# Performance work log

Hardware: AMD Instinct MI355X
Metric: run time of the kernel (lower is better)

Reference implementation:

```python
import jax, jax.numpy as jnp
import numpy as np

B, C, H = 16, 256, 32          # batch, in_channels(=out_channels), image_size
HEADS, HS = 8, 32              # heads = out_channels // head_size
D = HEADS * HS                 # head_dim = 256
N = H * H                      # tokens = 1024
EPS = 1e-5


def _rel_indices(h, w):
    # Faithful port of RelativeAttention2d.get_indices
    y = np.arange(h)
    x = np.arange(w)
    y1, x1, y2, x2 = np.meshgrid(y, x, y, x, indexing='ij')
    idx = (y1 - y2 + h - 1) * (2 * w - 1) + (x1 - x2 + w - 1)
    return jnp.asarray(idx.reshape(-1), dtype=jnp.int32)  # [N*N]


def setup_inputs() -> dict:
    key = jax.random.key(0)
    ks = jax.random.split(key, 10)
    s = 0.02
    return {
        'x': jax.random.normal(ks[0], (B, C, H, H), jnp.float32),
        'ln_g': jnp.ones((C,), jnp.float32),
        'ln_b': jnp.zeros((C,), jnp.float32),
        'wq': jax.random.normal(ks[1], (D, C), jnp.float32) * s,
        'bq': jnp.zeros((D,), jnp.float32),
        'wk': jax.random.normal(ks[2], (D, C), jnp.float32) * s,
        'bk': jnp.zeros((D,), jnp.float32),
        'wv': jax.random.normal(ks[3], (D, C), jnp.float32) * s,
        'bv': jnp.zeros((D,), jnp.float32),
        'wo': jax.random.normal(ks[4], (C, D), jnp.float32) * s,
        'bo': jnp.zeros((C,), jnp.float32),
        'rel_bias': jax.random.normal(ks[5], (HEADS, (2 * H - 1) * (2 * H - 1)), jnp.float32),
        'rel_idx': _rel_indices(H, H),
    }


def reference(x, ln_g, ln_b, wq, bq, wk, bk, wv, bv, wo, bo, rel_bias, rel_idx):
    b = x.shape[0]
    # norm(): LayerNorm over channel axis (dim 1 after the double transpose)
    mu = jnp.mean(x, axis=1, keepdims=True)
    var = jnp.mean((x - mu) ** 2, axis=1, keepdims=True)
    xn = (x - mu) / jnp.sqrt(var + EPS)
    xn = xn * ln_g[None, :, None, None] + ln_b[None, :, None, None]
    # reshape_for_linear: raw reshape [b, C, H, W] -> [b, N, C] (as in torch)
    xr = xn.reshape(b, N, C)
    # projections, then raw view(b, heads, head_size, -1) as in torch
    q = (xr @ wq.T + bq).reshape(b, HEADS, HS, N)
    k = (xr @ wk.T + bk).reshape(b, HEADS, HS, N)
    v = (xr @ wv.T + bv).reshape(b, HEADS, HS, N)
    # dots = k^T q / sqrt(head_dim)   [b, heads, N, N]
    dots = jnp.einsum('bhdn,bhdm->bhnm', k, q) / np.float32(np.sqrt(D))
    # gathered relative position bias  [heads, N, N]
    bias = rel_bias[:, rel_idx].reshape(HEADS, N, N)
    attn = jax.nn.softmax(dots + bias[None], axis=-2)  # non-standard softmax dim
    # out = v @ attn  [b, heads, head_size, N]
    out = jnp.einsum('bhdn,bhnm->bhdm', v, attn)
    out = out.reshape(b, H, H, D)  # raw view as in torch
    out = out @ wo.T + bo          # to_output linear (dropout is identity in eval)
    out = out.reshape(b, C, H, H)  # raw view back to [b, out_channels, H, W]
    return x + out
```

## Files before the change

kernel.cpp:

```cpp
#include <hip/hip_runtime.h>
#include <cstdint>

#define PERB 262144

typedef __attribute__((ext_vector_type(8))) short bf16x8;
typedef __attribute__((ext_vector_type(4))) float f32x4;
typedef unsigned short ushort_t;

__device__ __forceinline__ uint16_t f2bf(float f) {
    uint32_t u = __float_as_uint(f);
    u += 0x7fff + ((u >> 16) & 1);
    return (uint16_t)(u >> 16);
}

__global__ __launch_bounds__(256) void wcvt_kernel(
    const float* __restrict__ wq, const float* __restrict__ wk,
    const float* __restrict__ wv, const float* __restrict__ wo,
    ushort_t* __restrict__ oq, ushort_t* __restrict__ ok,
    ushort_t* __restrict__ ov, ushort_t* __restrict__ oo)
{
    const int which = blockIdx.x >> 6;
    const int idx = ((blockIdx.x & 63) * 256 + threadIdx.x) * 4;
    const float* src = which == 0 ? wq : which == 1 ? wk : which == 2 ? wv : wo;
    ushort_t* dst    = which == 0 ? oq : which == 1 ? ok : which == 2 ? ov : oo;
    const float4 v = *(const float4*)&src[idx];
    uint2 p;
    p.x = (uint32_t)f2bf(v.x) | ((uint32_t)f2bf(v.y) << 16);
    p.y = (uint32_t)f2bf(v.z) | ((uint32_t)f2bf(v.w) << 16);
    *(uint2*)&dst[idx] = p;
}

__global__ __launch_bounds__(256) void ln_kernel(
    const float* __restrict__ x, const float* __restrict__ gam,
    const float* __restrict__ bet, ushort_t* __restrict__ X)
{
    const int blk = blockIdx.x;
    const int b   = blk >> 4;
    const int sp0 = (blk & 15) << 6;
    const int tid = threadIdx.x;
    const int spl = tid & 63;
    const int cg  = tid >> 6;
    const int c0  = cg << 6;
    const int sp  = sp0 + spl;
    const float* xb = x + (size_t)b * PERB + sp;

    float vals[64];
    float s = 0.f, sq = 0.f;
#pragma unroll
    for (int i = 0; i < 64; ++i) {
        float v = xb[(size_t)(c0 + i) * 1024];
        vals[i] = v; s += v; sq += v * v;
    }
    __shared__ float rs[4][64];
    __shared__ float rq[4][64];
    rs[cg][spl] = s; rq[cg][spl] = sq;
    __syncthreads();
    const float ts = rs[0][spl] + rs[1][spl] + rs[2][spl] + rs[3][spl];
    const float tq = rq[0][spl] + rq[1][spl] + rq[2][spl] + rq[3][spl];
    const float mean = ts * (1.f / 256.f);
    const float var  = tq * (1.f / 256.f) - mean * mean;
    const float rstd = rsqrtf(var + 1e-5f);

    ushort_t* Xb = X + (size_t)b * PERB + sp;
#pragma unroll
    for (int i = 0; i < 64; ++i) {
        const int c = c0 + i;
        Xb[(size_t)c * 1024] = f2bf((vals[i] - mean) * rstd * gam[c] + bet[c]);
    }
}

__global__ __launch_bounds__(256, 3) void qkv_kernel(
    const ushort_t* __restrict__ X,
    const ushort_t* __restrict__ wq, const float* __restrict__ bq,
    const ushort_t* __restrict__ wk, const float* __restrict__ bk,
    const ushort_t* __restrict__ wv, const float* __restrict__ bv,
    ushort_t* __restrict__ Q, ushort_t* __restrict__ K, ushort_t* __restrict__ V)
{
    __shared__ __align__(16) ushort_t Xl[512 * 8];
    __shared__ __align__(16) ushort_t Wl[3][512 * 8];

    const int blk = blockIdx.x;
    const int m0  = (blk >> 2) << 6;
    const int n0  = (blk & 3) << 6;
    const int tid = threadIdx.x;
    const int w    = tid >> 6;
    const int lane = tid & 63;
    const int quad = lane >> 4;
    const int c    = lane & 15;

    f32x4 acc[3][4];
#pragma unroll
    for (int o3 = 0; o3 < 3; ++o3)
#pragma unroll
        for (int i = 0; i < 4; ++i) acc[o3][i] = (f32x4){0.f, 0.f, 0.f, 0.f};

    for (int kc = 0; kc < 4; ++kc) {
        const int k0 = kc << 6;
        __syncthreads();
#pragma unroll
        for (int i = 0; i < 2; ++i) {
            const int id = tid + i * 256;
            const int kq = id >> 6, m = id & 63;
            *(bf16x8*)&Xl[id * 8] = *(const bf16x8*)&X[(size_t)(m0 + m) * 256 + k0 + kq * 8];
        }
#pragma unroll
        for (int i = 0; i < 2; ++i) {
            const int id = tid + i * 256;
            const int kq = id >> 6, n = id & 63;
            const size_t g = (size_t)(n0 + n) * 256 + k0 + kq * 8;
            *(bf16x8*)&Wl[0][id * 8] = *(const bf16x8*)&wq[g];
            *(bf16x8*)&Wl[1][id * 8] = *(const bf16x8*)&wk[g];
            *(bf16x8*)&Wl[2][id * 8] = *(const bf16x8*)&wv[g];
        }
        __syncthreads();
#pragma unroll
        for (int ks = 0; ks < 2; ++ks) {
            const int kq = ks * 4 + quad;
            bf16x8 af[4];
#pragma unroll
            for (int msub = 0; msub < 4; ++msub)
                af[msub] = *(const bf16x8*)&Xl[(kq * 64 + msub * 16 + c) * 8];
            bf16x8 bw[3];
#pragma unroll
            for (int o3 = 0; o3 < 3; ++o3)
                bw[o3] = *(const bf16x8*)&Wl[o3][(kq * 64 + w * 16 + c) * 8];
#pragma unroll
            for (int o3 = 0; o3 < 3; ++o3)
#pragma unroll
                for (int msub = 0; msub < 4; ++msub)
                    acc[o3][msub] = __builtin_amdgcn_mfma_f32_16x16x32_bf16(
                        bw[o3], af[msub], acc[o3][msub], 0, 0, 0);
        }
    }

    const int n = n0 + w * 16 + quad * 4;
    const float4 bq4 = *(const float4*)&bq[n];
    const float4 bk4 = *(const float4*)&bk[n];
    const float4 bv4 = *(const float4*)&bv[n];
    ushort_t* outs[3] = {Q, K, V};
    const float4 bias[3] = {bq4, bk4, bv4};
#pragma unroll
    for (int msub = 0; msub < 4; ++msub) {
        const size_t m = (size_t)(m0 + msub * 16 + c);
#pragma unroll
        for (int o3 = 0; o3 < 3; ++o3) {
            const f32x4 a = acc[o3][msub];
            uint2 p;
            p.x = (uint32_t)f2bf(a[0] + bias[o3].x) | ((uint32_t)f2bf(a[1] + bias[o3].y) << 16);
            p.y = (uint32_t)f2bf(a[2] + bias[o3].z) | ((uint32_t)f2bf(a[3] + bias[o3].w) << 16);
            *(uint2*)&outs[o3][m * 256 + n] = p;
        }
    }
}

#define C1F 0.09016844005556022f
#define LOG2EF 1.4426950408889634f

__global__ __launch_bounds__(256, 4) void attn_kernel(
    const ushort_t* __restrict__ Q, const ushort_t* __restrict__ K,
    const ushort_t* __restrict__ V, const float* __restrict__ relb,
    ushort_t* __restrict__ O)
{
    __shared__ __align__(16) unsigned char smem[28672];
    char* Pb = (char*)smem;
    char* Kl = (char*)(smem + 16384);
    char* Vl = (char*)(smem + 20480);

    const int blk = blockIdx.x;
    const int bh  = blk & 127;
    const int mt  = blk >> 7;
    const int b   = bh >> 3;
    const int h   = bh & 7;
    const int m0  = mt << 7;
    const int tid = threadIdx.x;
    const int w    = tid >> 6;
    const int lane = tid & 63;
    const int quad = lane >> 4;
    const int c    = lane & 15;

    const size_t base = (size_t)b * PERB + (size_t)h * 32768;
    const ushort_t* Qg = Q + base;
    const ushort_t* Kg = K + base;
    const ushort_t* Vg = V + base;
    const float* rbh = relb + h * 3969;

    {
        const int mm = tid & 127;
        const int sg = tid >> 7;
        union { bf16x8 v; uint16_t u[8]; } g0, g1;
#pragma unroll
        for (int j = 0; j < 8; ++j)
            g0.u[j] = Qg[(size_t)(sg * 16 + j) * 1024 + m0 + mm];
#pragma unroll
        for (int j = 0; j < 8; ++j)
            g1.u[j] = Qg[(size_t)(sg * 16 + 8 + j) * 1024 + m0 + mm];
        *(bf16x8*)(Pb + (sg * 2 + 0) * 2048 + mm * 16) = g0.v;
        *(bf16x8*)(Pb + (sg * 2 + 1) * 2048 + mm * 16) = g1.v;
    }
    __syncthreads();
    bf16x8 qfrag[8];
#pragma unroll
    for (int msub = 0; msub < 8; ++msub)
        qfrag[msub] = *(const bf16x8*)(Pb + quad * 2048 + (msub * 16 + c) * 16);

    int moff[8];
#pragma unroll
    for (int msub = 0; msub < 8; ++msub) {
        const int m = m0 + msub * 16 + c;
        moff[msub] = 1984 - (m >> 5) * 63 - (m & 31);
    }

    f32x4 oacc[2][2], dacc[2];
#pragma unroll
    for (int i = 0; i < 2; ++i) {
        dacc[i] = (f32x4){0.f, 0.f, 0.f, 0.f};
#pragma unroll
        for (int j = 0; j < 2; ++j) oacc[i][j] = (f32x4){0.f, 0.f, 0.f, 0.f};
    }
    bf16x8 onesf;
#pragma unroll
    for (int j = 0; j < 8; ++j) onesf[j] = (short)0x3F80;

    const int knn = tid & 63, ksg = tid >> 6;
    const int vs  = tid >> 3, vng = tid & 7;
    const int kWr = ksg * 1024 + knn * 16;
    const int vWr = vs * 128 + ((vng ^ (vs & 7)) << 4);
    const int kRd = quad * 1024 + (w * 16 + c) * 16;
    const int pWr = c * 128 + (((2 * w + (quad >> 1)) ^ (c & 7)) << 4) + ((quad & 1) << 3);
    const int c7  = c & 7;

    uint32_t kpre[8]; bf16x8 vpre;
#pragma unroll
    for (int j = 0; j < 8; ++j) kpre[j] = Kg[(size_t)(ksg * 8 + j) * 1024 + knn];
    vpre = *(const bf16x8*)&Vg[(size_t)vs * 1024 + vng * 8];

    for (int ch = 0; ch < 16; ++ch) {
        const int n0c = ch << 6;
        const int cb  = ch & 1;

        {
            uint4 kp;
            kp.x = kpre[0] | (kpre[1] << 16);
            kp.y = kpre[2] | (kpre[3] << 16);
            kp.z = kpre[4] | (kpre[5] << 16);
            kp.w = kpre[6] | (kpre[7] << 16);
            *(uint4*)(Kl + kWr) = kp;
            *(bf16x8*)(Vl + cb * 4096 + vWr) = vpre;
        }
        __syncthreads();

        {
            const int n0n = ((ch + 1) & 15) << 6;
#pragma unroll
            for (int j = 0; j < 8; ++j)
                kpre[j] = Kg[(size_t)(ksg * 8 + j) * 1024 + n0n + knn];
            vpre = *(const bf16x8*)&Vg[(size_t)vs * 1024 + n0n + vng * 8];
        }

        const bf16x8 kf = *(const bf16x8*)(Kl + kRd);
        f32x4 sacc[8];
#pragma unroll
        for (int msub = 0; msub < 8; ++msub) {
            const f32x4 z = {0.f, 0.f, 0.f, 0.f};
            sacc[msub] = __builtin_amdgcn_mfma_f32_16x16x32_bf16(kf, qfrag[msub], z, 0, 0, 0);
        }

        const int nbase = n0c + w * 16 + quad * 4;
        const int nidx0 = (nbase >> 5) * 63 + (nbase & 31);
#pragma unroll
        for (int msub = 0; msub < 8; ++msub) {
            const float* bp = rbh + nidx0 + moff[msub];
            float p[4];
#pragma unroll
            for (int r = 0; r < 4; ++r)
                p[r] = __builtin_amdgcn_exp2f(fmaf(bp[r], LOG2EF, sacc[msub][r] * C1F));
            uint2 pk;
            pk.x = __builtin_amdgcn_perm(__float_as_uint(p[1]), __float_as_uint(p[0]), 0x07060302u);
            pk.y = __builtin_amdgcn_perm(__float_as_uint(p[3]), __float_as_uint(p[2]), 0x07060302u);
            *(uint2*)(Pb + msub * 2048 + pWr) = pk;
        }
        __syncthreads();

#pragma unroll
        for (int kstep = 0; kstep < 2; ++kstep) {
            const int u = ((kstep * 4 + quad) ^ c7) << 4;
            const bf16x8 vf0 = *(const bf16x8*)(Vl + cb * 4096 + c * 128 + u);
            const bf16x8 vf1 = *(const bf16x8*)(Vl + cb * 4096 + (16 + c) * 128 + u);
#pragma unroll
            for (int mi = 0; mi < 2; ++mi) {
                const bf16x8 pf = *(const bf16x8*)(Pb + ((w * 2 + mi) * 16 + c) * 128 + u);
                oacc[0][mi] = __builtin_amdgcn_mfma_f32_16x16x32_bf16(vf0, pf, oacc[0][mi], 0, 0, 0);
                oacc[1][mi] = __builtin_amdgcn_mfma_f32_16x16x32_bf16(vf1, pf, oacc[1][mi], 0, 0, 0);
                dacc[mi]    = __builtin_amdgcn_mfma_f32_16x16x32_bf16(onesf, pf, dacc[mi], 0, 0, 0);
            }
        }
    }

    ushort_t* Ob = O + base;
#pragma unroll
    for (int mi = 0; mi < 2; ++mi) {
        const float inv = 1.0f / dacc[mi][0];
        const int m = m0 + (w * 2 + mi) * 16 + c;
#pragma unroll
        for (int ssub = 0; ssub < 2; ++ssub)
#pragma unroll
            for (int r = 0; r < 4; ++r)
                Ob[(size_t)(ssub * 16 + quad * 4 + r) * 1024 + m] = f2bf(oacc[ssub][mi][r] * inv);
    }
}

__global__ __launch_bounds__(256, 4) void oproj_kernel(
    const ushort_t* __restrict__ A, const ushort_t* __restrict__ wo,
    const float* __restrict__ bo, const float* __restrict__ x,
    float* __restrict__ out)
{
    __shared__ __align__(16) ushort_t Al[512 * 8];
    __shared__ __align__(16) ushort_t Wl[512 * 8];

    const int blk = blockIdx.x;
    const int m0  = (blk >> 2) << 6;
    const int n0  = (blk & 3) << 6;
    const int tid = threadIdx.x;
    const int w    = tid >> 6;
    const int lane = tid & 63;
    const int quad = lane >> 4;
    const int c    = lane & 15;

    f32x4 acc[4];
#pragma unroll
    for (int i = 0; i < 4; ++i) acc[i] = (f32x4){0.f, 0.f, 0.f, 0.f};

    for (int kc = 0; kc < 4; ++kc) {
        const int k0 = kc << 6;
        __syncthreads();
#pragma unroll
        for (int i = 0; i < 2; ++i) {
            const int id = tid + i * 256;
            const int kq = id >> 6, mn = id & 63;
            *(bf16x8*)&Al[id * 8] = *(const bf16x8*)&A [(size_t)(m0 + mn) * 256 + k0 + kq * 8];
            *(bf16x8*)&Wl[id * 8] = *(const bf16x8*)&wo[(size_t)(n0 + mn) * 256 + k0 + kq * 8];
        }
        __syncthreads();
#pragma unroll
        for (int ks = 0; ks < 2; ++ks) {
            const int kq = ks * 4 + quad;
            const bf16x8 bw = *(const bf16x8*)&Wl[(kq * 64 + w * 16 + c) * 8];
#pragma unroll
            for (int msub = 0; msub < 4; ++msub) {
                const bf16x8 af = *(const bf16x8*)&Al[(kq * 64 + msub * 16 + c) * 8];
                acc[msub] = __builtin_amdgcn_mfma_f32_16x16x32_bf16(bw, af, acc[msub], 0, 0, 0);
            }
        }
    }

    const int n = n0 + w * 16 + quad * 4;
    const float4 bo4 = *(const float4*)&bo[n];
#pragma unroll
    for (int msub = 0; msub < 4; ++msub) {
        const size_t g = (size_t)(m0 + msub * 16 + c) * 256 + n;
        const float4 r = *(const float4*)&x[g];
        float4 t;
        t.x = acc[msub][0] + bo4.x + r.x;
        t.y = acc[msub][1] + bo4.y + r.y;
        t.z = acc[msub][2] + bo4.z + r.z;
        t.w = acc[msub][3] + bo4.w + r.w;
        *(float4*)&out[g] = t;
    }
}

extern "C" void kernel_launch(void* const* d_in, const int* in_sizes, int n_in,
                              void* d_out, int out_size, void* d_ws, size_t ws_size,
                              hipStream_t stream)
{
    (void)in_sizes; (void)n_in; (void)out_size; (void)ws_size;
    const float* x   = (const float*)d_in[0];
    const float* lng = (const float*)d_in[1];
    const float* lnb = (const float*)d_in[2];
    const float* wq  = (const float*)d_in[3];
    const float* bq  = (const float*)d_in[4];
    const float* wk  = (const float*)d_in[5];
    const float* bk  = (const float*)d_in[6];
    const float* wv  = (const float*)d_in[7];
    const float* bv  = (const float*)d_in[8];
    const float* wo  = (const float*)d_in[9];
    const float* bo  = (const float*)d_in[10];
    const float* rb  = (const float*)d_in[11];

    ushort_t* ws = (ushort_t*)d_ws;
    ushort_t* Xbf = ws;
    ushort_t* Qbf = ws + 1 * 4194304;
    ushort_t* Kbf = ws + 2 * 4194304;
    ushort_t* Vbf = ws + 3 * 4194304;
    ushort_t* Obf = ws + 4 * 4194304;
    ushort_t* Wqb = ws + 5 * 4194304;
    ushort_t* Wkb = Wqb + 65536;
    ushort_t* Wvb = Wkb + 65536;
    ushort_t* Wob = Wvb + 65536;
    float* out = (float*)d_out;

    hipLaunchKernelGGL(wcvt_kernel,  dim3(256),  dim3(256), 0, stream,
                       wq, wk, wv, wo, Wqb, Wkb, Wvb, Wob);
    hipLaunchKernelGGL(ln_kernel,    dim3(256),  dim3(256), 0, stream, x, lng, lnb, Xbf);
    hipLaunchKernelGGL(qkv_kernel,   dim3(1024), dim3(256), 0, stream,
                       Xbf, Wqb, bq, Wkb, bk, Wvb, bv, Qbf, Kbf, Vbf);
    hipLaunchKernelGGL(attn_kernel,  dim3(1024), dim3(256), 0, stream, Qbf, Kbf, Vbf, rb, Obf);
    hipLaunchKernelGGL(oproj_kernel, dim3(1024), dim3(256), 0, stream, Obf, Wob, bo, x, out);
}
```

Before: 179.2 us.

## Merge weight-convert and layernorm kernels; halve attention query tile to double grid

Fuses the weight bf16 conversion and the layernorm into one prep kernel, saving a launch. The layernorm now uses 512 smaller blocks of 32 spatial positions × 8 channel groups, giving more parallelism. The attention kernel now handles 64 queries per block instead of 128, which doubles the grid to 2048 blocks and shrinks LDS and register use. The cost is that each K/V chunk is loaded and staged twice as often per query, and the per-chunk barriers are amortised over less MFMA work.

Measured after the change: 176.7 us. No clear change (-1.4%).

```diff
diff --git a/kernel.cpp b/kernel.cpp
--- a/kernel.cpp
+++ b/kernel.cpp
@@ -13,59 +13,60 @@
     return (uint16_t)(u >> 16);
 }
 
-__global__ __launch_bounds__(256) void wcvt_kernel(
+__global__ __launch_bounds__(256) void prep_kernel(
+    const float* __restrict__ x, const float* __restrict__ gam,
+    const float* __restrict__ bet, ushort_t* __restrict__ X,
     const float* __restrict__ wq, const float* __restrict__ wk,
     const float* __restrict__ wv, const float* __restrict__ wo,
     ushort_t* __restrict__ oq, ushort_t* __restrict__ ok,
     ushort_t* __restrict__ ov, ushort_t* __restrict__ oo)
 {
-    const int which = blockIdx.x >> 6;
-    const int idx = ((blockIdx.x & 63) * 256 + threadIdx.x) * 4;
-    const float* src = which == 0 ? wq : which == 1 ? wk : which == 2 ? wv : wo;
-    ushort_t* dst    = which == 0 ? oq : which == 1 ? ok : which == 2 ? ov : oo;
-    const float4 v = *(const float4*)&src[idx];
-    uint2 p;
-    p.x = (uint32_t)f2bf(v.x) | ((uint32_t)f2bf(v.y) << 16);
-    p.y = (uint32_t)f2bf(v.z) | ((uint32_t)f2bf(v.w) << 16);
-    *(uint2*)&dst[idx] = p;
-}
-
-__global__ __launch_bounds__(256) void ln_kernel(
-    const float* __restrict__ x, const float* __restrict__ gam,
-    const float* __restrict__ bet, ushort_t* __restrict__ X)
-{
     const int blk = blockIdx.x;
-    const int b   = blk >> 4;
-    const int sp0 = (blk & 15) << 6;
     const int tid = threadIdx.x;
-    const int spl = tid & 63;
-    const int cg  = tid >> 6;
-    const int c0  = cg << 6;
+    if (blk < 256) {
+        const int which = blk >> 6;
+        const int idx = ((blk & 63) * 256 + tid) * 4;
+        const float* src = which == 0 ? wq : which == 1 ? wk : which == 2 ? wv : wo;
+        ushort_t* dst    = which == 0 ? oq : which == 1 ? ok : which == 2 ? ov : oo;
+        const float4 v = *(const float4*)&src[idx];
+        uint2 p;
+        p.x = (uint32_t)f2bf(v.x) | ((uint32_t)f2bf(v.y) << 16);
+        p.y = (uint32_t)f2bf(v.z) | ((uint32_t)f2bf(v.w) << 16);
+        *(uint2*)&dst[idx] = p;
+        return;
+    }
+    const int lb  = blk - 256;
+    const int b   = lb >> 5;
+    const int sp0 = (lb & 31) << 5;
+    const int spl = tid & 31;
+    const int cg  = tid >> 5;
+    const int c0  = cg << 5;
     const int sp  = sp0 + spl;
     const float* xb = x + (size_t)b * PERB + sp;
 
-    float vals[64];
+    float vals[32];
     float s = 0.f, sq = 0.f;
 #pragma unroll
-    for (int i = 0; i < 64; ++i) {
+    for (int i = 0; i < 32; ++i) {
         float v = xb[(size_t)(c0 + i) * 1024];
         vals[i] = v; s += v; sq += v * v;
     }
-    __shared__ float rs[4][64];
-    __shared__ float rq[4][64];
+    __shared__ float rs[8][32];
+    __shared__ float rq[8][32];
     rs[cg][spl] = s; rq[cg][spl] = sq;
     __syncthreads();
-    const float ts = rs[0][spl] + rs[1][spl] + rs[2][spl] + rs[3][spl];
-    const float tq = rq[0][spl] + rq[1][spl] + rq[2][spl] + rq[3][spl];
+    float ts = 0.f, tq = 0.f;
+#pragma unroll
+    for (int g = 0; g < 8; ++g) { ts += rs[g][spl]; tq += rq[g][spl]; }
     const float mean = ts * (1.f / 256.f);
     const float var  = tq * (1.f / 256.f) - mean * mean;
     const float rstd = rsqrtf(var + 1e-5f);
 
     ushort_t* Xb = X + (size_t)b * PERB + sp;
 #pragma unroll
-    for (int i = 0; i < 64; ++i) {
-        const int c = c0 + i;
-        Xb[(size_t)c * 1024] = f2bf((vals[i] - mean) * rstd * gam[c] + bet[c]);
+    for (int i = 0; i < 32; ++i) {
+        const int cc = c0 + i;
+        Xb[(size_t)cc * 1024] = f2bf((vals[i] - mean) * rstd * gam[cc] + bet[cc]);
     }
 }
 
@@ -161,17 +162,17 @@
     const ushort_t* __restrict__ V, const float* __restrict__ relb,
     ushort_t* __restrict__ O)
 {
-    __shared__ __align__(16) unsigned char smem[28672];
+    __shared__ __align__(16) unsigned char smem[20480];
     char* Pb = (char*)smem;
-    char* Kl = (char*)(smem + 16384);
-    char* Vl = (char*)(smem + 20480);
+    char* Kl = (char*)(smem + 8192);
+    char* Vl = (char*)(smem + 12288);
 
     const int blk = blockIdx.x;
     const int bh  = blk & 127;
     const int mt  = blk >> 7;
     const int b   = bh >> 3;
     const int h   = bh & 7;
-    const int m0  = mt << 7;
+    const int m0  = mt << 6;
     const int tid = threadIdx.x;
     const int w    = tid >> 6;
     const int lane = tid & 63;
@@ -185,38 +186,31 @@
     const float* rbh = relb + h * 3969;
 
     {
-        const int mm = tid & 127;
-        const int sg = tid >> 7;
-        union { bf16x8 v; uint16_t u[8]; } g0, g1;
+        const int mm = tid & 63;
+        const int sg = tid >> 6;
+        union { bf16x8 v; uint16_t u[8]; } g0;
 #pragma unroll
         for (int j = 0; j < 8; ++j)
-            g0.u[j] = Qg[(size_t)(sg * 16 + j) * 1024 + m0 + mm];
-#pragma unroll
-        for (int j = 0; j < 8; ++j)
-            g1.u[j] = Qg[(size_t)(sg * 16 + 8 + j) * 1024 + m0 + mm];
-        *(bf16x8*)(Pb + (sg * 2 + 0) * 2048 + mm * 16) = g0.v;
-        *(bf16x8*)(Pb + (sg * 2 + 1) * 2048 + mm * 16) = g1.v;
+            g0.u[j] = Qg[(size_t)(sg * 8 + j) * 1024 + m0 + mm];
+        *(bf16x8*)(Pb + sg * 1024 + mm * 16) = g0.v;
     }
     __syncthreads();
-    bf16x8 qfrag[8];
-#pragma unroll
-    for (int msub = 0; msub < 8; ++msub)
-        qfrag[msub] = *(const bf16x8*)(Pb + quad * 2048 + (msub * 16 + c) * 16);
-
-    int moff[8];
-#pragma unroll
-    for (int msub = 0; msub < 8; ++msub) {
+    bf16x8 qfrag[4];
+#pragma unroll
+    for (int msub = 0; msub < 4; ++msub)
+        qfrag[msub] = *(const bf16x8*)(Pb + quad * 1024 + (msub * 16 + c) * 16);
+
+    int moff[4];
+#pragma unroll
+    for (int msub = 0; msub < 4; ++msub) {
         const int m = m0 + msub * 16 + c;
         moff[msub] = 1984 - (m >> 5) * 63 - (m & 31);
     }
 
-    f32x4 oacc[2][2], dacc[2];
-#pragma unroll
-    for (int i = 0; i < 2; ++i) {
-        dacc[i] = (f32x4){0.f, 0.f, 0.f, 0.f};
-#pragma unroll
-        for (int j = 0; j < 2; ++j) oacc[i][j] = (f32x4){0.f, 0.f, 0.f, 0.f};
-    }
+    f32x4 oacc[2], dacc;
+    dacc = (f32x4){0.f, 0.f, 0.f, 0.f};
+#pragma unroll
+    for (int j = 0; j < 2; ++j) oacc[j] = (f32x4){0.f, 0.f, 0.f, 0.f};
     bf16x8 onesf;
 #pragma unroll
     for (int j = 0; j < 8; ++j) onesf[j] = (short)0x3F80;
@@ -258,9 +252,9 @@
         }
 
         const bf16x8 kf = *(const bf16x8*)(Kl + kRd);
-        f32x4 sacc[8];
-#pragma unroll
-        for (int msub = 0; msub < 8; ++msub) {
+        f32x4 sacc[4];
+#pragma unroll
+        for (int msub = 0; msub < 4; ++msub) {
             const f32x4 z = {0.f, 0.f, 0.f, 0.f};
             sacc[msub] = __builtin_amdgcn_mfma_f32_16x16x32_bf16(kf, qfrag[msub], z, 0, 0, 0);
         }
@@ -268,7 +262,7 @@
         const int nbase = n0c + w * 16 + quad * 4;
         const int nidx0 = (nbase >> 5) * 63 + (nbase & 31);
 #pragma unroll
-        for (int msub = 0; msub < 8; ++msub) {
+        for (int msub = 0; msub < 4; ++msub) {
             const float* bp = rbh + nidx0 + moff[msub];
             float p[4];
 #pragma unroll
@@ -286,27 +280,21 @@
             const int u = ((kstep * 4 + quad) ^ c7) << 4;
             const bf16x8 vf0 = *(const bf16x8*)(Vl + cb * 4096 + c * 128 + u);
             const bf16x8 vf1 = *(const bf16x8*)(Vl + cb * 4096 + (16 + c) * 128 + u);
-#pragma unroll
-            for (int mi = 0; mi < 2; ++mi) {
-                const bf16x8 pf = *(const bf16x8*)(Pb + ((w * 2 + mi) * 16 + c) * 128 + u);
-                oacc[0][mi] = __builtin_amdgcn_mfma_f32_16x16x32_bf16(vf0, pf, oacc[0][mi], 0, 0, 0);
-                oacc[1][mi] = __builtin_amdgcn_mfma_f32_16x16x32_bf16(vf1, pf, oacc[1][mi], 0, 0, 0);
-                dacc[mi]    = __builtin_amdgcn_mfma_f32_16x16x32_bf16(onesf, pf, dacc[mi], 0, 0, 0);
-            }
+            const bf16x8 pf  = *(const bf16x8*)(Pb + (w * 16 + c) * 128 + u);
+            oacc[0] = __builtin_amdgcn_mfma_f32_16x16x32_bf16(vf0, pf, oacc[0], 0, 0, 0);
+            oacc[1] = __builtin_amdgcn_mfma_f32_16x16x32_bf16(vf1, pf, oacc[1], 0, 0, 0);
+            dacc    = __builtin_amdgcn_mfma_f32_16x16x32_bf16(onesf, pf, dacc, 0, 0, 0);
         }
     }
 
     ushort_t* Ob = O + base;
-#pragma unroll
-    for (int mi = 0; mi < 2; ++mi) {
-        const float inv = 1.0f / dacc[mi][0];
-        const int m = m0 + (w * 2 + mi) * 16 + c;
-#pragma unroll
-        for (int ssub = 0; ssub < 2; ++ssub)
-#pragma unroll
-            for (int r = 0; r < 4; ++r)
-                Ob[(size_t)(ssub * 16 + quad * 4 + r) * 1024 + m] = f2bf(oacc[ssub][mi][r] * inv);
-    }
+    const float inv = 1.0f / dacc[0];
+    const int m = m0 + w * 16 + c;
+#pragma unroll
+    for (int ssub = 0; ssub < 2; ++ssub)
+#pragma unroll
+        for (int r = 0; r < 4; ++r)
+            Ob[(size_t)(ssub * 16 + quad * 4 + r) * 1024 + m] = f2bf(oacc[ssub][r] * inv);
 }
 
 __global__ __launch_bounds__(256, 4) void oproj_kernel(
@@ -398,11 +386,10 @@
     ushort_t* Wob = Wvb + 65536;
     float* out = (float*)d_out;
 
-    hipLaunchKernelGGL(wcvt_kernel,  dim3(256),  dim3(256), 0, stream,
-                       wq, wk, wv, wo, Wqb, Wkb, Wvb, Wob);
-    hipLaunchKernelGGL(ln_kernel,    dim3(256),  dim3(256), 0, stream, x, lng, lnb, Xbf);
+    hipLaunchKernelGGL(prep_kernel,  dim3(768),  dim3(256), 0, stream,
+                       x, lng, lnb, Xbf, wq, wk, wv, wo, Wqb, Wkb, Wvb, Wob);
     hipLaunchKernelGGL(qkv_kernel,   dim3(1024), dim3(256), 0, stream,
                        Xbf, Wqb, bq, Wkb, bk, Wvb, bv, Qbf, Kbf, Vbf);
-    hipLaunchKernelGGL(attn_kernel,  dim3(1024), dim3(256), 0, stream, Qbf, Kbf, Vbf, rb, Obf);
+    hipLaunchKernelGGL(attn_kernel,  dim3(2048), dim3(256), 0, stream, Qbf, Kbf, Vbf, rb, Obf);
     hipLaunchKernelGGL(oproj_kernel, dim3(1024), dim3(256), 0, stream, Obf, Wob, bo, x, out);
 }
```

## Double-buffer QKV and output GEMMs with direct global-to-LDS loads; merge prep kernels

Applied to the files above, without the earlier changes.

The QKV and output-projection GEMMs now stage tiles straight into LDS with global_load_lds, using an XOR-swizzled layout and two LDS buffers so the next K-chunk loads while the current one computes. Each K iteration needs one barrier instead of two. The weight conversion and LayerNorm kernels are merged into one launch, and LayerNorm is retiled to more, smaller blocks for higher occupancy. In exchange the QKV kernel uses twice as much LDS, which may reduce resident blocks, and its occupancy hint in launch_bounds is removed.

New measurement: 161.2 us. 10.0% less time.

```diff
diff --git a/kernel.cpp b/kernel.cpp
--- a/kernel.cpp
+++ b/kernel.cpp
@@ -13,71 +13,124 @@
     return (uint16_t)(u >> 16);
 }
 
-__global__ __launch_bounds__(256) void wcvt_kernel(
+__device__ __forceinline__ void glds16(const void* g, void* l) {
+    __builtin_amdgcn_global_load_lds(
+        (const __attribute__((address_space(1))) void*)g,
+        (__attribute__((address_space(3))) void*)l, 16, 0, 0);
+}
+
+__global__ __launch_bounds__(256) void prep_kernel(
+    const float* __restrict__ x, const float* __restrict__ gam,
+    const float* __restrict__ bet, ushort_t* __restrict__ X,
     const float* __restrict__ wq, const float* __restrict__ wk,
     const float* __restrict__ wv, const float* __restrict__ wo,
     ushort_t* __restrict__ oq, ushort_t* __restrict__ ok,
     ushort_t* __restrict__ ov, ushort_t* __restrict__ oo)
 {
-    const int which = blockIdx.x >> 6;
-    const int idx = ((blockIdx.x & 63) * 256 + threadIdx.x) * 4;
-    const float* src = which == 0 ? wq : which == 1 ? wk : which == 2 ? wv : wo;
-    ushort_t* dst    = which == 0 ? oq : which == 1 ? ok : which == 2 ? ov : oo;
-    const float4 v = *(const float4*)&src[idx];
-    uint2 p;
-    p.x = (uint32_t)f2bf(v.x) | ((uint32_t)f2bf(v.y) << 16);
-    p.y = (uint32_t)f2bf(v.z) | ((uint32_t)f2bf(v.w) << 16);
-    *(uint2*)&dst[idx] = p;
-}
-
-__global__ __launch_bounds__(256) void ln_kernel(
-    const float* __restrict__ x, const float* __restrict__ gam,
-    const float* __restrict__ bet, ushort_t* __restrict__ X)
-{
     const int blk = blockIdx.x;
-    const int b   = blk >> 4;
-    const int sp0 = (blk & 15) << 6;
     const int tid = threadIdx.x;
-    const int spl = tid & 63;
-    const int cg  = tid >> 6;
-    const int c0  = cg << 6;
+    if (blk < 256) {
+        const int which = blk >> 6;
+        const int idx = ((blk & 63) * 256 + tid) * 4;
+        const float* src = which == 0 ? wq : which == 1 ? wk : which == 2 ? wv : wo;
+        ushort_t* dst    = which == 0 ? oq : which == 1 ? ok : which == 2 ? ov : oo;
+        const float4 v = *(const float4*)&src[idx];
+        uint2 p;
+        p.x = (uint32_t)f2bf(v.x) | ((uint32_t)f2bf(v.y) << 16);
+        p.y = (uint32_t)f2bf(v.z) | ((uint32_t)f2bf(v.w) << 16);
+        *(uint2*)&dst[idx] = p;
+        return;
+    }
+    const int lb  = blk - 256;
+    const int b   = lb >> 5;
+    const int sp0 = (lb & 31) << 5;
+    const int spl = tid & 31;
+    const int cg  = tid >> 5;
+    const int c0  = cg << 5;
     const int sp  = sp0 + spl;
     const float* xb = x + (size_t)b * PERB + sp;
 
-    float vals[64];
+    float vals[32];
     float s = 0.f, sq = 0.f;
 #pragma unroll
-    for (int i = 0; i < 64; ++i) {
+    for (int i = 0; i < 32; ++i) {
         float v = xb[(size_t)(c0 + i) * 1024];
         vals[i] = v; s += v; sq += v * v;
     }
-    __shared__ float rs[4][64];
-    __shared__ float rq[4][64];
+    __shared__ float rs[8][32];
+    __shared__ float rq[8][32];
     rs[cg][spl] = s; rq[cg][spl] = sq;
     __syncthreads();
-    const float ts = rs[0][spl] + rs[1][spl] + rs[2][spl] + rs[3][spl];
-    const float tq = rq[0][spl] + rq[1][spl] + rq[2][spl] + rq[3][spl];
+    float ts = 0.f, tq = 0.f;
+#pragma unroll
+    for (int g = 0; g < 8; ++g) { ts += rs[g][spl]; tq += rq[g][spl]; }
     const float mean = ts * (1.f / 256.f);
     const float var  = tq * (1.f / 256.f) - mean * mean;
     const float rstd = rsqrtf(var + 1e-5f);
 
     ushort_t* Xb = X + (size_t)b * PERB + sp;
 #pragma unroll
-    for (int i = 0; i < 64; ++i) {
-        const int c = c0 + i;
-        Xb[(size_t)c * 1024] = f2bf((vals[i] - mean) * rstd * gam[c] + bet[c]);
-    }
-}
-
-__global__ __launch_bounds__(256, 3) void qkv_kernel(
+    for (int i = 0; i < 32; ++i) {
+        const int cc = c0 + i;
+        Xb[(size_t)cc * 1024] = f2bf((vals[i] - mean) * rstd * gam[cc] + bet[cc]);
+    }
+}
+
+__device__ __forceinline__ void qkv_stage(
+    ushort_t* Sb, const ushort_t* __restrict__ X,
+    const ushort_t* __restrict__ wq, const ushort_t* __restrict__ wk,
+    const ushort_t* __restrict__ wv,
+    int m0, int n0, int k0, int w, int lane)
+{
+    const int rsub = lane >> 3;
+    const int u    = lane & 7;
+    const int koct = u ^ rsub;
+#pragma unroll
+    for (int i = 0; i < 2; ++i) {
+        const int rg  = w * 2 + i;
+        const int row = rg * 8 + rsub;
+        const int go  = k0 + koct * 8;
+        ushort_t* db = Sb + rg * 512;
+        glds16(&X [(size_t)(m0 + row) * 256 + go], db);
+        glds16(&wq[(size_t)(n0 + row) * 256 + go], db + 4096);
+        glds16(&wk[(size_t)(n0 + row) * 256 + go], db + 8192);
+        glds16(&wv[(size_t)(n0 + row) * 256 + go], db + 12288);
+    }
+}
+
+__device__ __forceinline__ void qkv_compute(
+    const ushort_t* Sb, int w, int c, int quad, f32x4 acc[3][4])
+{
+#pragma unroll
+    for (int ks = 0; ks < 2; ++ks) {
+        const int kq = ks * 4 + quad;
+        const int uo = (kq ^ (c & 7)) * 8;
+        bf16x8 af[4];
+#pragma unroll
+        for (int msub = 0; msub < 4; ++msub)
+            af[msub] = *(const bf16x8*)&Sb[(msub * 16 + c) * 64 + uo];
+        bf16x8 bw[3];
+#pragma unroll
+        for (int o3 = 0; o3 < 3; ++o3)
+            bw[o3] = *(const bf16x8*)&Sb[(o3 + 1) * 4096 + (w * 16 + c) * 64 + uo];
+#pragma unroll
+        for (int o3 = 0; o3 < 3; ++o3)
+#pragma unroll
+            for (int msub = 0; msub < 4; ++msub)
+                acc[o3][msub] = __builtin_amdgcn_mfma_f32_16x16x32_bf16(
+                    bw[o3], af[msub], acc[o3][msub], 0, 0, 0);
+    }
+}
+
+__global__ __launch_bounds__(256) void qkv_kernel(
     const ushort_t* __restrict__ X,
     const ushort_t* __restrict__ wq, const float* __restrict__ bq,
     const ushort_t* __restrict__ wk, const float* __restrict__ bk,
     const ushort_t* __restrict__ wv, const float* __restrict__ bv,
     ushort_t* __restrict__ Q, ushort_t* __restrict__ K, ushort_t* __restrict__ V)
 {
-    __shared__ __align__(16) ushort_t Xl[512 * 8];
-    __shared__ __align__(16) ushort_t Wl[3][512 * 8];
+    __shared__ __align__(16) ushort_t SB0[4][4096];
+    __shared__ __align__(16) ushort_t SB1[4][4096];
 
     const int blk = blockIdx.x;
     const int m0  = (blk >> 2) << 6;
@@ -94,43 +147,19 @@
 #pragma unroll
         for (int i = 0; i < 4; ++i) acc[o3][i] = (f32x4){0.f, 0.f, 0.f, 0.f};
 
+    qkv_stage(&SB0[0][0], X, wq, wk, wv, m0, n0, 0, w, lane);
+    __syncthreads();
+#pragma unroll
     for (int kc = 0; kc < 4; ++kc) {
-        const int k0 = kc << 6;
+        if (kc < 3) {
+            if ((kc & 1) == 0)
+                qkv_stage(&SB1[0][0], X, wq, wk, wv, m0, n0, (kc + 1) << 6, w, lane);
+            else
+                qkv_stage(&SB0[0][0], X, wq, wk, wv, m0, n0, (kc + 1) << 6, w, lane);
+        }
+        if ((kc & 1) == 0) qkv_compute(&SB0[0][0], w, c, quad, acc);
+        else               qkv_compute(&SB1[0][0], w, c, quad, acc);
         __syncthreads();
-#pragma unroll
-        for (int i = 0; i < 2; ++i) {
-            const int id = tid + i * 256;
-            const int kq = id >> 6, m = id & 63;
-            *(bf16x8*)&Xl[id * 8] = *(const bf16x8*)&X[(size_t)(m0 + m) * 256 + k0 + kq * 8];
-        }
-#pragma unroll
-        for (int i = 0; i < 2; ++i) {
-            const int id = tid + i * 256;
-            const int kq = id >> 6, n = id & 63;
-            const size_t g = (size_t)(n0 + n) * 256 + k0 + kq * 8;
-            *(bf16x8*)&Wl[0][id * 8] = *(const bf16x8*)&wq[g];
-            *(bf16x8*)&Wl[1][id * 8] = *(const bf16x8*)&wk[g];
-            *(bf16x8*)&Wl[2][id * 8] = *(const bf16x8*)&wv[g];
-        }
-        __syncthreads();
-#pragma unroll
-        for (int ks = 0; ks < 2; ++ks) {
-            const int kq = ks * 4 + quad;
-            bf16x8 af[4];
-#pragma unroll
-            for (int msub = 0; msub < 4; ++msub)
-                af[msub] = *(const bf16x8*)&Xl[(kq * 64 + msub * 16 + c) * 8];
-            bf16x8 bw[3];
-#pragma unroll
-            for (int o3 = 0; o3 < 3; ++o3)
-                bw[o3] = *(const bf16x8*)&Wl[o3][(kq * 64 + w * 16 + c) * 8];
-#pragma unroll
-            for (int o3 = 0; o3 < 3; ++o3)
-#pragma unroll
-                for (int msub = 0; msub < 4; ++msub)
-                    acc[o3][msub] = __builtin_amdgcn_mfma_f32_16x16x32_bf16(
-                        bw[o3], af[msub], acc[o3][msub], 0, 0, 0);
-        }
     }
 
     const int n = n0 + w * 16 + quad * 4;
@@ -309,13 +338,47 @@
     }
 }
 
+__device__ __forceinline__ void oproj_stage(
+    ushort_t* Sb, const ushort_t* __restrict__ A, const ushort_t* __restrict__ wo,
+    int m0, int n0, int k0, int w, int lane)
+{
+    const int rsub = lane >> 3;
+    const int u    = lane & 7;
+    const int koct = u ^ rsub;
+#pragma unroll
+    for (int i = 0; i < 2; ++i) {
+        const int rg  = w * 2 + i;
+        const int row = rg * 8 + rsub;
+        const int go  = k0 + koct * 8;
+        ushort_t* db = Sb + rg * 512;
+        glds16(&A [(size_t)(m0 + row) * 256 + go], db);
+        glds16(&wo[(size_t)(n0 + row) * 256 + go], db + 4096);
+    }
+}
+
+__device__ __forceinline__ void oproj_compute(
+    const ushort_t* Sb, int w, int c, int quad, f32x4 acc[4])
+{
+#pragma unroll
+    for (int ks = 0; ks < 2; ++ks) {
+        const int kq = ks * 4 + quad;
+        const int uo = (kq ^ (c & 7)) * 8;
+        const bf16x8 bw = *(const bf16x8*)&Sb[4096 + (w * 16 + c) * 64 + uo];
+#pragma unroll
+        for (int msub = 0; msub < 4; ++msub) {
+            const bf16x8 af = *(const bf16x8*)&Sb[(msub * 16 + c) * 64 + uo];
+            acc[msub] = __builtin_amdgcn_mfma_f32_16x16x32_bf16(bw, af, acc[msub], 0, 0, 0);
+        }
+    }
+}
+
 __global__ __launch_bounds__(256, 4) void oproj_kernel(
     const ushort_t* __restrict__ A, const ushort_t* __restrict__ wo,
     const float* __restrict__ bo, const float* __restrict__ x,
     float* __restrict__ out)
 {
-    __shared__ __align__(16) ushort_t Al[512 * 8];
-    __shared__ __align__(16) ushort_t Wl[512 * 8];
+    __shared__ __align__(16) ushort_t SA0[2][4096];
+    __shared__ __align__(16) ushort_t SA1[2][4096];
 
     const int blk = blockIdx.x;
     const int m0  = (blk >> 2) << 6;
@@ -330,27 +393,19 @@
 #pragma unroll
     for (int i = 0; i < 4; ++i) acc[i] = (f32x4){0.f, 0.f, 0.f, 0.f};
 
+    oproj_stage(&SA0[0][0], A, wo, m0, n0, 0, w, lane);
+    __syncthreads();
+#pragma unroll
     for (int kc = 0; kc < 4; ++kc) {
-        const int k0 = kc << 6;
+        if (kc < 3) {
+            if ((kc & 1) == 0)
+                oproj_stage(&SA1[0][0], A, wo, m0, n0, (kc + 1) << 6, w, lane);
+            else
+                oproj_stage(&SA0[0][0], A, wo, m0, n0, (kc + 1) << 6, w, lane);
+        }
+        if ((kc & 1) == 0) oproj_compute(&SA0[0][0], w, c, quad, acc);
+        else               oproj_compute(&SA1[0][0], w, c, quad, acc);
         __syncthreads();
-#pragma unroll
-        for (int i = 0; i < 2; ++i) {
-            const int id = tid + i * 256;
-            const int kq = id >> 6, mn = id & 63;
-            *(bf16x8*)&Al[id * 8] = *(const bf16x8*)&A [(size_t)(m0 + mn) * 256 + k0 + kq * 8];
-            *(bf16x8*)&Wl[id * 8] = *(const bf16x8*)&wo[(size_t)(n0 + mn) * 256 + k0 + kq * 8];
-        }
-        __syncthreads();
-#pragma unroll
-        for (int ks = 0; ks < 2; ++ks) {
-            const int kq = ks * 4 + quad;
-            const bf16x8 bw = *(const bf16x8*)&Wl[(kq * 64 + w * 16 + c) * 8];
-#pragma unroll
-            for (int msub = 0; msub < 4; ++msub) {
-                const bf16x8 af = *(const bf16x8*)&Al[(kq * 64 + msub * 16 + c) * 8];
-                acc[msub] = __builtin_amdgcn_mfma_f32_16x16x32_bf16(bw, af, acc[msub], 0, 0, 0);
-            }
-        }
     }
 
     const int n = n0 + w * 16 + quad * 4;
@@ -398,9 +453,8 @@
     ushort_t* Wob = Wvb + 65536;
     float* out = (float*)d_out;
 
-    hipLaunchKernelGGL(wcvt_kernel,  dim3(256),  dim3(256), 0, stream,
-                       wq, wk, wv, wo, Wqb, Wkb, Wvb, Wob);
-    hipLaunchKernelGGL(ln_kernel,    dim3(256),  dim3(256), 0, stream, x, lng, lnb, Xbf);
+    hipLaunchKernelGGL(prep_kernel,  dim3(768),  dim3(256), 0, stream,
+                       x, lng, lnb, Xbf, wq, wk, wv, wo, Wqb, Wkb, Wvb, Wob);
     hipLaunchKernelGGL(qkv_kernel,   dim3(1024), dim3(256), 0, stream,
                        Xbf, Wqb, bq, Wkb, bk, Wvb, bv, Qbf, Kbf, Vbf);
     hipLaunchKernelGGL(attn_kernel,  dim3(1024), dim3(256), 0, stream, Qbf, Kbf, Vbf, rb, Obf);
```
